# Performance work log

Hardware: AMD Instinct MI355X
Metric: run time of the kernel (lower is better)

The kernel has to match this reference:

```python
import jax, jax.numpy as jnp
import numpy as np

T, B, C = 2000, 32, 128   # frames, batch, classes (blank = 0)
L = 100                   # target length (fixed per batch)
W0, WLAST, THALF, NSTEP = 1.0, 0.1, 10000.0, 1
NEG_INF = -1e30

# ---- static STC graph (star-augmented CTC lattice) ----
# states: 0..2L  standard CTC lattice (even=blank, odd=target[(l-1)//2])
#         2L+1+l star node c_l for l=0..L  -> N = 3L+2
# arc label types: 0=blank, 1=target[lpos], 2=star_minus_target[lpos] (idx C+tgt), 3=full star (idx C)
# arc weight types: 0 -> 0, 1 -> log(wt), 2 -> 0 if target[wpos]!=target[wpos-1] else -inf (skip arc)

def _build_arcs(L):
    S = 2 * L + 1
    star = lambda l: S + l
    rows = []
    add = lambda s, d, lt, lp, wt, wp: rows.append((s, d, lt, lp, wt, wp))
    for l in range(S):
        idx = (l - 1) // 2
        if l % 2 == 0:
            add(l, l, 0, 0, 0, 0)              # blank self-loop
        if l > 0:
            if l % 2:
                add(l - 1, l, 1, idx, 0, 0)    # advance, emit target[idx]
            else:
                add(l - 1, l, 0, 0, 0, 0)      # advance, emit blank
        if l % 2 and l > 1:
            add(l - 2, l, 1, idx, 2, idx)      # skip arc (masked on repeats)
    for l in range(L + 1):
        p1, p2, c1 = 2 * l - 1, 2 * l, star(l)
        lt, lp = (3, 0) if l == L else (2, l)
        if p1 >= 0:
            add(p1, c1, lt, lp, 1, 0)
        add(p2, c1, lt, lp, 1, 0)
        add(c1, c1, lt, lp, 1, 0)              # star self-loop, weight log(wt)
        if l < L:
            add(c1, 2 * l + 1, 1, l, 0, 0)
        add(c1, p2, 0, 0, 0, 0)
    a = np.array(rows, dtype=np.int32).T
    return tuple(jnp.asarray(x) for x in a)

SRC, DST, LTYPE, LPOS, WTYPE, WPOS = _build_arcs(L)
N_STATES = 3 * L + 2
ACCEPT = jnp.array([2 * L - 1, 2 * L, 3 * L + 1])  # S-2, S-1, star c_L


def setup_inputs():
    key = jax.random.key(0)
    k1, k2 = jax.random.split(key)
    logits = jax.random.normal(k1, (T, B, C), dtype=jnp.float32)
    inputs = jax.nn.log_softmax(logits, axis=-1)          # [T, B, C] log-probs
    targets = jax.random.randint(k2, (B, L), 1, C, dtype=jnp.int32)
    return {"inputs": inputs, "targets": targets}


def _stc_loss(lp_aug, targets, logwt):
    # lp_aug: [B, T, 2C] augmented emissions; targets: [B, L]
    tgt = targets[:, LPOS]                                   # [B, A]
    labels = jnp.where(LTYPE == 0, 0,
             jnp.where(LTYPE == 1, tgt,
             jnp.where(LTYPE == 2, C + tgt, C)))             # [B, A] emission index
    prev = targets[:, jnp.maximum(WPOS - 1, 0)]
    w = jnp.where(WTYPE == 0, 0.0,
        jnp.where(WTYPE == 1, logwt,
        jnp.where(targets[:, WPOS] != prev, 0.0, NEG_INF)))  # [B, A]
    alpha0 = jnp.full((B, N_STATES), NEG_INF, dtype=lp_aug.dtype).at[:, 0].set(0.0)

    seg_max = jax.vmap(lambda s: jax.ops.segment_max(s, DST, num_segments=N_STATES))
    seg_sum = jax.vmap(lambda s: jax.ops.segment_sum(s, DST, num_segments=N_STATES))

    def step(alpha, emit_t):                                 # emit_t: [B, 2C]
        sc = alpha[:, SRC] + w + jnp.take_along_axis(emit_t, labels, axis=1)
        m = jnp.maximum(seg_max(sc), NEG_INF)                # stable scatter-logsumexp
        z = seg_sum(jnp.exp(sc - m[:, DST]))
        return m + jnp.log(z), None

    alpha, _ = jax.lax.scan(step, alpha0, jnp.swapaxes(lp_aug, 0, 1))
    score = jax.nn.logsumexp(alpha[:, ACCEPT], axis=1)       # forward score
    return jnp.mean(-score / T)                              # reduction='mean' then batch mean


def reference(inputs, targets):
    # wt schedule (nstep = 1 after one training step)
    wt = WLAST + (W0 - WLAST) * np.exp(-NSTEP * np.log(2.0) / THALF)
    lp = jnp.transpose(inputs, (1, 0, 2))                    # [B, T, C]
    lse = jax.nn.logsumexp(lp[:, :, 1:], axis=2, keepdims=True)
    neglse = lse + jnp.log1p(1e-7 - jnp.exp(lp[:, :, 1:] - lse))  # logsubexp
    lp_aug = jnp.concatenate([lp, lse, neglse], axis=2)      # [B, T, 2C]
    return _stc_loss(lp_aug, targets, float(np.log(wt)))
```

## Files before the change

### kernel.cpp

```cpp
#include <hip/hip_runtime.h>
#include <math.h>


#define T_LEN   2000
#define BATCH   32
#define NCLS    128
#define LTGT    100
#define CHUNK   16
#define EROWS   8
#define NEG_INF_F (-1e30f)

typedef float f32x4 __attribute__((ext_vector_type(4)));

#if __has_builtin(__builtin_amdgcn_exp2f)
#define EXP2(x) __builtin_amdgcn_exp2f(x)
#else
#define EXP2(x) exp2f(x)
#endif
#if __has_builtin(__builtin_amdgcn_logf)
#define LOG2(x) __builtin_amdgcn_logf(x)
#else
#define LOG2(x) __log2f(x)
#endif

__global__ void __launch_bounds__(64)
stc_emit(const float* __restrict__ inputs,
         const int*   __restrict__ targets,
         float4*      __restrict__ tabA,
         float*       __restrict__ tabB,
         const float wt)
{
    const int tbase = blockIdx.x * EROWS;
    const int b     = blockIdx.y;
    const int lane  = threadIdx.x;

    __shared__ float lps[EROWS][NCLS];

    int tg0 = 0, tg1 = 0;
    if (lane < 50) {
        tg0 = targets[b * LTGT + 2 * lane];
        tg1 = targets[b * LTGT + 2 * lane + 1];
    }
    const float L2E = 1.4426950408889634f;

#define ELD(i) const float2 x##i = *(const float2*)(inputs +                 \
                   ((size_t)(tbase + (i)) * BATCH + b) * NCLS + 2 * lane);
    ELD(0) ELD(1) ELD(2) ELD(3) ELD(4) ELD(5) ELD(6) ELD(7)
#undef ELD
#define EST(i) *(float2*)&lps[i][2 * lane] = x##i;
    EST(0) EST(1) EST(2) EST(3) EST(4) EST(5) EST(6) EST(7)
#undef EST
#define EPART(i) const float ex##i = __expf(x##i.x);                          \
                 float p##i = (lane == 0) ? __expf(x##i.y)                    \
                                          : ex##i + __expf(x##i.y);
    EPART(0) EPART(1) EPART(2) EPART(3) EPART(4) EPART(5) EPART(6) EPART(7)
#undef EPART
#define ERED(off) p0 += __shfl_xor(p0, off, 64); p1 += __shfl_xor(p1, off, 64);\
                  p2 += __shfl_xor(p2, off, 64); p3 += __shfl_xor(p3, off, 64);\
                  p4 += __shfl_xor(p4, off, 64); p5 += __shfl_xor(p5, off, 64);\
                  p6 += __shfl_xor(p6, off, 64); p7 += __shfl_xor(p7, off, 64);
    ERED(32) ERED(16) ERED(8) ERED(4) ERED(2) ERED(1)
#undef ERED
#define EPB(i) const float pb##i = __shfl(ex##i, 0, 64);
    EPB(0) EPB(1) EPB(2) EPB(3) EPB(4) EPB(5) EPB(6) EPB(7)
#undef EPB

    if (lane < 50) {
#define EOUT(i) do {                                                          \
        const float lt0 = lps[i][tg0], lt1 = lps[i][tg1];                     \
        const float aa  = fmaf(wt * (1.0f + 1e-7f), p##i, pb##i);             \
        const float q0  = fmaf(-wt, __expf(lt0), aa);                         \
        const float q1  = fmaf(-wt, __expf(lt1), aa);                         \
        tabA[((size_t)b * T_LEN + tbase + (i)) * 50 + lane] =                 \
            make_float4(L2E * lt0, L2E * lt1, LOG2(q0), LOG2(q1));            \
    } while (0);
        EOUT(0) EOUT(1) EOUT(2) EOUT(3) EOUT(4) EOUT(5) EOUT(6) EOUT(7)
#undef EOUT
    } else if (lane == 50) {
#define EOB(i) tabB[(size_t)b * T_LEN + tbase + (i)] =                        \
                   LOG2(fmaf(wt, p##i, pb##i));
        EOB(0) EOB(1) EOB(2) EOB(3) EOB(4) EOB(5) EOB(6) EOB(7)
#undef EOB
    }
}

__device__ __forceinline__ float shift_up1_ninf(float x)
{
    return __int_as_float(
        __builtin_amdgcn_update_dpp(__float_as_int(NEG_INF_F),
                                    __float_as_int(x), 0x138, 0xf, 0xf, false));
}
__device__ __forceinline__ float shift_dn1_ninf(float x)
{
    return __int_as_float(
        __builtin_amdgcn_update_dpp(__float_as_int(NEG_INF_F),
                                    __float_as_int(x), 0x130, 0xf, 0xf, false));
}

#define GL4(dst, base, imm)                                             \
    asm volatile("global_load_dwordx4 %0, %1, off offset:" #imm         \
                 : "=&v"(dst) : "v"(base))
#define VMWAIT(n) do {                                                  \
        asm volatile("s_waitcnt vmcnt(" #n ")" ::: "memory");           \
        __builtin_amdgcn_sched_barrier(0);                              \
    } while (0)

__global__ void __launch_bounds__(128, 1)
stc_scan(const float4* __restrict__ tabA,
         const float*  __restrict__ tabB,
         const int*    __restrict__ targets,
         float*        __restrict__ out)
{
    const int b    = blockIdx.x;
    const int lane = threadIdx.x & 63;
    const int wave = threadIdx.x >> 6;
    const bool l50 = (lane == 50);

    __shared__ float sb[4][64];

    const int tb0 = b * LTGT;
    const int c0 = 2 * lane, c1 = 2 * lane + 1;
    bool skb0 = false, skb1 = false;
    if (c0 >= 1 && c0 <= 99)
        skb0 = (targets[tb0 + c0] != targets[tb0 + c0 - 1]);
    if (c1 <= 99)
        skb1 = (targets[tb0 + c1] != targets[tb0 + c1 - 1]);

    const char* gAc = (const char*)tabA + (size_t)b * T_LEN * 800
                    + (size_t)lane * 16;
    const char* gQc = (const char*)(tabB + (size_t)b * T_LEN);

    asm volatile("s_waitcnt vmcnt(0) lgkmcnt(0)" ::: "memory");
    __builtin_amdgcn_sched_barrier(0);

    f32x4 Xv0, Xv1, Xv2, Xv3, Xv4, Xv5, Xv6, Xv7,
          Xv8, Xv9, Xv10, Xv11, Xv12, Xv13, Xv14, Xv15, Xq0, Xq1, Xq2, Xq3;
    f32x4 Yv0, Yv1, Yv2, Yv3, Yv4, Yv5, Yv6, Yv7,
          Yv8, Yv9, Yv10, Yv11, Yv12, Yv13, Yv14, Yv15, Yq0, Yq1, Yq2, Yq3;

#define LOADB(P, trow) do {                                             \
        const char* a0_ = gAc + (size_t)(trow) * 800;                   \
        const char* a1_ = a0_ + 4000;                                   \
        const char* a2_ = a0_ + 8000;                                   \
        GL4(P##v0,  a0_, 0);    GL4(P##v1,  a0_, 800);                  \
        GL4(P##v2,  a0_, 1600); GL4(P##v3,  a0_, 2400);                 \
        GL4(P##v4,  a0_, 3200);                                         \
        GL4(P##v5,  a1_, 0);    GL4(P##v6,  a1_, 800);                  \
        GL4(P##v7,  a1_, 1600); GL4(P##v8,  a1_, 2400);                 \
        GL4(P##v9,  a1_, 3200);                                         \
        GL4(P##v10, a2_, 0);    GL4(P##v11, a2_, 800);                  \
        GL4(P##v12, a2_, 1600); GL4(P##v13, a2_, 2400);                 \
        GL4(P##v14, a2_, 3200); GL4(P##v15, a2_, 4000);                 \
        const char* q_ = gQc + (size_t)(trow) * 4;                      \
        GL4(P##q0, q_, 0);  GL4(P##q1, q_, 16);                         \
        GL4(P##q2, q_, 32); GL4(P##q3, q_, 48);                         \
    } while (0)

    float A0 = (lane == 0) ? 0.0f : NEG_INF_F;
    float O0 = NEG_INF_F, A1 = NEG_INF_F, O1 = NEG_INF_F;
    float p0 = NEG_INF_F;

    if (wave == 0) {
#define FSTEP(vx, vy, vz, vw, qk) do {                                 \
        const float m1  = fmaxf(A1, O0);                               \
        const float lz1 = LOG2(1.0f + EXP2(-fabsf(A1 - O0)));          \
        const float O1n = skb1 ? (m1 + (vy)) + lz1 : A1 + (vy);        \
        const float psh = shift_up1_ninf(O1n);                         \
        A1 = (m1 + (vw)) + lz1;                                        \
        O1 = O1n;                                                      \
        const float m0  = fmaxf(A0, p0);                               \
        const float lz0 = LOG2(1.0f + EXP2(-fabsf(A0 - p0)));          \
        const float lq0 = l50 ? (qk) : (vz);                           \
        O0 = skb0 ? (m0 + (vx)) + lz0 : A0 + (vx);                     \
        A0 = (m0 + lq0) + lz0;                                         \
        p0 = psh;                                                      \
    } while (0)
#define RUNF(P) do {                                                       \
        FSTEP(P##v0[0],  P##v0[1],  P##v0[2],  P##v0[3],  P##q0[0]);       \
        FSTEP(P##v1[0],  P##v1[1],  P##v1[2],  P##v1[3],  P##q0[1]);       \
        FSTEP(P##v2[0],  P##v2[1],  P##v2[2],  P##v2[3],  P##q0[2]);       \
        FSTEP(P##v3[0],  P##v3[1],  P##v3[2],  P##v3[3],  P##q0[3]);       \
        FSTEP(P##v4[0],  P##v4[1],  P##v4[2],  P##v4[3],  P##q1[0]);       \
        FSTEP(P##v5[0],  P##v5[1],  P##v5[2],  P##v5[3],  P##q1[1]);       \
        FSTEP(P##v6[0],  P##v6[1],  P##v6[2],  P##v6[3],  P##q1[2]);       \
        FSTEP(P##v7[0],  P##v7[1],  P##v7[2],  P##v7[3],  P##q1[3]);       \
        FSTEP(P##v8[0],  P##v8[1],  P##v8[2],  P##v8[3],  P##q2[0]);       \
        FSTEP(P##v9[0],  P##v9[1],  P##v9[2],  P##v9[3],  P##q2[1]);       \
        FSTEP(P##v10[0], P##v10[1], P##v10[2], P##v10[3], P##q2[2]);       \
        FSTEP(P##v11[0], P##v11[1], P##v11[2], P##v11[3], P##q2[3]);       \
        FSTEP(P##v12[0], P##v12[1], P##v12[2], P##v12[3], P##q3[0]);       \
        FSTEP(P##v13[0], P##v13[1], P##v13[2], P##v13[3], P##q3[1]);       \
        FSTEP(P##v14[0], P##v14[1], P##v14[2], P##v14[3], P##q3[2]);       \
        FSTEP(P##v15[0], P##v15[1], P##v15[2], P##v15[3], P##q3[3]);       \
    } while (0)
        LOADB(X, 0);
        for (int c = 0; c + 1 < 63; c += 2) {
            LOADB(Y, 16 * (c + 1)); VMWAIT(20); RUNF(X);
            LOADB(X, 16 * (c + 2)); VMWAIT(20); RUNF(Y);
        }
        VMWAIT(0); RUNF(X);
#undef RUNF
#undef FSTEP
    } else {
        float bA0 = l50 ? 0.0f : NEG_INF_F;
        float bA1 = NEG_INF_F;
        float bO0 = NEG_INF_F;
        float bO1 = (lane == 49) ? 0.0f : NEG_INF_F;
#define BSTEP(vx, vy, vz, vw, qk) do {                                 \
        const float x1  = bA1 + (vw);                                  \
        const float y1  = bO1 + (vy);                                  \
        const float m1  = fmaxf(x1, y1);                               \
        const float lz1 = LOG2(1.0f + EXP2(-fabsf(x1 - y1)));          \
        const float L1  = m1 + lz1;                                    \
        const float lq0 = l50 ? (qk) : (vz);                           \
        const float x0  = bA0 + lq0;                                   \
        const float y0  = bO0 + (vx);                                  \
        const float m0  = fmaxf(x0, y0);                               \
        const float lz0 = LOG2(1.0f + EXP2(-fabsf(x0 - y0)));          \
        const float L0  = m0 + lz0;                                    \
        const float t0  = skb0 ? L0 : x0;                              \
        const float psh = shift_dn1_ninf(t0);       \
        bO0 = skb1 ? L1 : x1;                                          \
        bA0 = l50 ? x0 : L0;                                           \
        bA1 = L1;                                                      \
        bO1 = psh;                                                     \
    } while (0)
#define RUNBK(P) do {                                                      \
        BSTEP(P##v15[0], P##v15[1], P##v15[2], P##v15[3], P##q3[3]);       \
        BSTEP(P##v14[0], P##v14[1], P##v14[2], P##v14[3], P##q3[2]);       \
        BSTEP(P##v13[0], P##v13[1], P##v13[2], P##v13[3], P##q3[1]);       \
        BSTEP(P##v12[0], P##v12[1], P##v12[2], P##v12[3], P##q3[0]);       \
        BSTEP(P##v11[0], P##v11[1], P##v11[2], P##v11[3], P##q2[3]);       \
        BSTEP(P##v10[0], P##v10[1], P##v10[2], P##v10[3], P##q2[2]);       \
        BSTEP(P##v9[0],  P##v9[1],  P##v9[2],  P##v9[3],  P##q2[1]);       \
        BSTEP(P##v8[0],  P##v8[1],  P##v8[2],  P##v8[3],  P##q2[0]);       \
        BSTEP(P##v7[0],  P##v7[1],  P##v7[2],  P##v7[3],  P##q1[3]);       \
        BSTEP(P##v6[0],  P##v6[1],  P##v6[2],  P##v6[3],  P##q1[2]);       \
        BSTEP(P##v5[0],  P##v5[1],  P##v5[2],  P##v5[3],  P##q1[1]);       \
        BSTEP(P##v4[0],  P##v4[1],  P##v4[2],  P##v4[3],  P##q1[0]);       \
        BSTEP(P##v3[0],  P##v3[1],  P##v3[2],  P##v3[3],  P##q0[3]);       \
        BSTEP(P##v2[0],  P##v2[1],  P##v2[2],  P##v2[3],  P##q0[2]);       \
        BSTEP(P##v1[0],  P##v1[1],  P##v1[2],  P##v1[3],  P##q0[1]);       \
        BSTEP(P##v0[0],  P##v0[1],  P##v0[2],  P##v0[3],  P##q0[0]);       \
    } while (0)
        LOADB(X, 1984);
        for (int k = 0; k + 1 < 61; k += 2) {
            LOADB(Y, 1984 - 16 * (k + 1)); VMWAIT(20); RUNBK(X);
            LOADB(X, 1984 - 16 * (k + 2)); VMWAIT(20); RUNBK(Y);
        }
        LOADB(Y, 1008); VMWAIT(20); RUNBK(X);
        VMWAIT(0); RUNBK(Y);
#undef RUNBK
#undef BSTEP
        sb[0][lane] = bA0; sb[1][lane] = bA1;
        sb[2][lane] = bO0; sb[3][lane] = bO1;
    }
#undef LOADB

    __syncthreads();

    if (wave == 0) {
        const float bA0g = sb[0][lane], bA1g = sb[1][lane];
        const float bO0g = sb[2][lane], bO1g = sb[3][lane];
        const float T0 = (lane <= 50) ? A0 + bA0g : NEG_INF_F;
        const float T1 = (lane < 50)  ? A1 + bA1g : NEG_INF_F;
        const float T2 = (lane < 50)  ? O0 + bO0g : NEG_INF_F;
        const float T3 = (lane < 50)  ? O1 + bO1g : NEG_INF_F;
        float M = fmaxf(fmaxf(T0, T1), fmaxf(T2, T3));
        float S = EXP2(T0 - M) + EXP2(T1 - M) + EXP2(T2 - M) + EXP2(T3 - M);
        #pragma unroll
        for (int off = 32; off >= 1; off >>= 1) {
            const float Mo = __shfl_xor(M, off, 64);
            const float So = __shfl_xor(S, off, 64);
            const float Mn = fmaxf(M, Mo);
            S = S * EXP2(M - Mn) + So * EXP2(Mo - Mn);
            M = Mn;
        }
        if (lane == 0) {
            const float LN2 = 0.6931471805599453f;
            atomicAdd(out, -(M + LOG2(S)) * LN2
                               / ((float)T_LEN * (float)BATCH));
        }
    }
}

extern "C" void kernel_launch(void* const* d_in, const int* in_sizes, int n_in,
                              void* d_out, int out_size, void* d_ws, size_t ws_size,
                              hipStream_t stream)
{
    const float* inputs  = (const float*)d_in[0];
    const int*   targets = (const int*)d_in[1];
    float*       out     = (float*)d_out;

    float4* tabA = (float4*)d_ws;
    float*  tabB = (float*)((char*)d_ws + (size_t)BATCH * T_LEN * 50 * 16);

    const float wt = (float)(0.1 + 0.9 * exp(-log(2.0) / 10000.0));

    (void)hipMemsetAsync(out, 0, sizeof(float), stream);
    stc_emit<<<dim3(T_LEN / EROWS, BATCH), dim3(64), 0, stream>>>(
        inputs, targets, tabA, tabB, wt);
    stc_scan<<<dim3(BATCH), dim3(128), 0, stream>>>(tabA, tabB, targets, out);
}
```

Baseline: 138.5 us.

## Fuse emission precompute into scan kernel with producer waves and LDS double buffer

The separate emission kernel and its global-memory tables are removed. A single 256-thread block per batch item now runs two producer waves, one per direction, that load raw log-probs, compute the augmented emissions, and write them into a double-buffered LDS staging area. Two consumer waves run the forward and backward recursions, reading their 16-step chunk from LDS. This avoids the second launch and the write and re-read of the large intermediate tables. In exchange it adds a block-wide barrier per chunk, and producer compute or load latency now sits on the critical path of the serial scan.

```diff
diff --git a/kernel.cpp b/kernel.cpp
--- a/kernel.cpp
+++ b/kernel.cpp
@@ -6,11 +6,10 @@
 #define BATCH   32
 #define NCLS    128
 #define LTGT    100
-#define CHUNK   16
-#define EROWS   8
 #define NEG_INF_F (-1e30f)
 
 typedef float f32x4 __attribute__((ext_vector_type(4)));
+typedef float f32x2 __attribute__((ext_vector_type(2)));
 
 #if __has_builtin(__builtin_amdgcn_exp2f)
 #define EXP2(x) __builtin_amdgcn_exp2f(x)
@@ -23,67 +22,6 @@
 #define LOG2(x) __log2f(x)
 #endif
 
-__global__ void __launch_bounds__(64)
-stc_emit(const float* __restrict__ inputs,
-         const int*   __restrict__ targets,
-         float4*      __restrict__ tabA,
-         float*       __restrict__ tabB,
-         const float wt)
-{
-    const int tbase = blockIdx.x * EROWS;
-    const int b     = blockIdx.y;
-    const int lane  = threadIdx.x;
-
-    __shared__ float lps[EROWS][NCLS];
-
-    int tg0 = 0, tg1 = 0;
-    if (lane < 50) {
-        tg0 = targets[b * LTGT + 2 * lane];
-        tg1 = targets[b * LTGT + 2 * lane + 1];
-    }
-    const float L2E = 1.4426950408889634f;
-
-#define ELD(i) const float2 x##i = *(const float2*)(inputs +                 \
-                   ((size_t)(tbase + (i)) * BATCH + b) * NCLS + 2 * lane);
-    ELD(0) ELD(1) ELD(2) ELD(3) ELD(4) ELD(5) ELD(6) ELD(7)
-#undef ELD
-#define EST(i) *(float2*)&lps[i][2 * lane] = x##i;
-    EST(0) EST(1) EST(2) EST(3) EST(4) EST(5) EST(6) EST(7)
-#undef EST
-#define EPART(i) const float ex##i = __expf(x##i.x);                          \
-                 float p##i = (lane == 0) ? __expf(x##i.y)                    \
-                                          : ex##i + __expf(x##i.y);
-    EPART(0) EPART(1) EPART(2) EPART(3) EPART(4) EPART(5) EPART(6) EPART(7)
-#undef EPART
-#define ERED(off) p0 += __shfl_xor(p0, off, 64); p1 += __shfl_xor(p1, off, 64);\
-                  p2 += __shfl_xor(p2, off, 64); p3 += __shfl_xor(p3, off, 64);\
-                  p4 += __shfl_xor(p4, off, 64); p5 += __shfl_xor(p5, off, 64);\
-                  p6 += __shfl_xor(p6, off, 64); p7 += __shfl_xor(p7, off, 64);
-    ERED(32) ERED(16) ERED(8) ERED(4) ERED(2) ERED(1)
-#undef ERED
-#define EPB(i) const float pb##i = __shfl(ex##i, 0, 64);
-    EPB(0) EPB(1) EPB(2) EPB(3) EPB(4) EPB(5) EPB(6) EPB(7)
-#undef EPB
-
-    if (lane < 50) {
-#define EOUT(i) do {                                                          \
-        const float lt0 = lps[i][tg0], lt1 = lps[i][tg1];                     \
-        const float aa  = fmaf(wt * (1.0f + 1e-7f), p##i, pb##i);             \
-        const float q0  = fmaf(-wt, __expf(lt0), aa);                         \
-        const float q1  = fmaf(-wt, __expf(lt1), aa);                         \
-        tabA[((size_t)b * T_LEN + tbase + (i)) * 50 + lane] =                 \
-            make_float4(L2E * lt0, L2E * lt1, LOG2(q0), LOG2(q1));            \
-    } while (0);
-        EOUT(0) EOUT(1) EOUT(2) EOUT(3) EOUT(4) EOUT(5) EOUT(6) EOUT(7)
-#undef EOUT
-    } else if (lane == 50) {
-#define EOB(i) tabB[(size_t)b * T_LEN + tbase + (i)] =                        \
-                   LOG2(fmaf(wt, p##i, pb##i));
-        EOB(0) EOB(1) EOB(2) EOB(3) EOB(4) EOB(5) EOB(6) EOB(7)
-#undef EOB
-    }
-}
-
 __device__ __forceinline__ float shift_up1_ninf(float x)
 {
     return __int_as_float(
@@ -97,25 +35,41 @@
                                     __float_as_int(x), 0x130, 0xf, 0xf, false));
 }
 
-#define GL4(dst, base, imm)                                             \
-    asm volatile("global_load_dwordx4 %0, %1, off offset:" #imm         \
+__device__ __forceinline__ unsigned ldsa(const void* p)
+{
+    return (unsigned)(unsigned long long)
+        (const __attribute__((address_space(3))) char*)p;
+}
+
+#define GL2(dst, base)                                                  \
+    asm volatile("global_load_dwordx2 %0, %1, off"                      \
                  : "=&v"(dst) : "v"(base))
+#define DSR4(dst, addr, imm)                                            \
+    asm volatile("ds_read_b128 %0, %1 offset:" #imm                     \
+                 : "=&v"(dst) : "v"(addr))
 #define VMWAIT(n) do {                                                  \
         asm volatile("s_waitcnt vmcnt(" #n ")" ::: "memory");           \
         __builtin_amdgcn_sched_barrier(0);                              \
     } while (0)
-
-__global__ void __launch_bounds__(128, 1)
-stc_scan(const float4* __restrict__ tabA,
-         const float*  __restrict__ tabB,
-         const int*    __restrict__ targets,
-         float*        __restrict__ out)
+#define LGKMWAIT() do {                                                 \
+        asm volatile("s_waitcnt lgkmcnt(0)" ::: "memory");              \
+        __builtin_amdgcn_sched_barrier(0);                              \
+    } while (0)
+
+__global__ void __launch_bounds__(256, 1)
+stc_fused(const float* __restrict__ inputs,
+          const int*   __restrict__ targets,
+          float*       __restrict__ out,
+          const float wt)
 {
     const int b    = blockIdx.x;
     const int lane = threadIdx.x & 63;
     const int wave = threadIdx.x >> 6;
     const bool l50 = (lane == 50);
 
+    __shared__ float4 emisA[2][2][16][64];
+    __shared__ __align__(16) float emisQ[2][2][16];
+    __shared__ float lps[2][16][NCLS];
     __shared__ float sb[4][64];
 
     const int tb0 = b * LTGT;
@@ -125,42 +79,122 @@
         skb0 = (targets[tb0 + c0] != targets[tb0 + c0 - 1]);
     if (c1 <= 99)
         skb1 = (targets[tb0 + c1] != targets[tb0 + c1 - 1]);
-
-    const char* gAc = (const char*)tabA + (size_t)b * T_LEN * 800
-                    + (size_t)lane * 16;
-    const char* gQc = (const char*)(tabB + (size_t)b * T_LEN);
-
-    asm volatile("s_waitcnt vmcnt(0) lgkmcnt(0)" ::: "memory");
-    __builtin_amdgcn_sched_barrier(0);
-
-    f32x4 Xv0, Xv1, Xv2, Xv3, Xv4, Xv5, Xv6, Xv7,
-          Xv8, Xv9, Xv10, Xv11, Xv12, Xv13, Xv14, Xv15, Xq0, Xq1, Xq2, Xq3;
-    f32x4 Yv0, Yv1, Yv2, Yv3, Yv4, Yv5, Yv6, Yv7,
-          Yv8, Yv9, Yv10, Yv11, Yv12, Yv13, Yv14, Yv15, Yq0, Yq1, Yq2, Yq3;
-
-#define LOADB(P, trow) do {                                             \
-        const char* a0_ = gAc + (size_t)(trow) * 800;                   \
-        const char* a1_ = a0_ + 4000;                                   \
-        const char* a2_ = a0_ + 8000;                                   \
-        GL4(P##v0,  a0_, 0);    GL4(P##v1,  a0_, 800);                  \
-        GL4(P##v2,  a0_, 1600); GL4(P##v3,  a0_, 2400);                 \
-        GL4(P##v4,  a0_, 3200);                                         \
-        GL4(P##v5,  a1_, 0);    GL4(P##v6,  a1_, 800);                  \
-        GL4(P##v7,  a1_, 1600); GL4(P##v8,  a1_, 2400);                 \
-        GL4(P##v9,  a1_, 3200);                                         \
-        GL4(P##v10, a2_, 0);    GL4(P##v11, a2_, 800);                  \
-        GL4(P##v12, a2_, 1600); GL4(P##v13, a2_, 2400);                 \
-        GL4(P##v14, a2_, 3200); GL4(P##v15, a2_, 4000);                 \
-        const char* q_ = gQc + (size_t)(trow) * 4;                      \
-        GL4(P##q0, q_, 0);  GL4(P##q1, q_, 16);                         \
-        GL4(P##q2, q_, 32); GL4(P##q3, q_, 48);                         \
-    } while (0)
+    int tg0 = 0, tg1 = 0;
+    if (lane < 50) {
+        tg0 = targets[tb0 + c0];
+        tg1 = targets[tb0 + c1];
+    }
+
+    const float L2E = 1.4426950408889634f;
+    const float wtp = wt * (1.0f + 1e-7f);
+    const char* inSrc = (const char*)inputs + (size_t)b * 512
+                      + (size_t)lane * 8;
+
+    {
+        const float4 z4 = make_float4(0.f, 0.f, 0.f, 0.f);
+        float4* ea = (float4*)emisA;
+        for (int i = threadIdx.x; i < 2 * 2 * 16 * 64; i += 256) ea[i] = z4;
+        float* eq = (float*)emisQ;
+        if (threadIdx.x < 64) eq[threadIdx.x] = 0.f;
+    }
+
+#define PTROW(dir, c) ((dir) ? (1984 - 16 * (c)) : (16 * (c)))
+#define LOADP(S, trow) do {                                             \
+        const char* p_ = inSrc + (size_t)(trow) * 16384;                \
+        GL2(S##0,  p_);            GL2(S##1,  p_ + 16384);              \
+        GL2(S##2,  p_ + 32768);    GL2(S##3,  p_ + 49152);              \
+        GL2(S##4,  p_ + 65536);    GL2(S##5,  p_ + 81920);              \
+        GL2(S##6,  p_ + 98304);    GL2(S##7,  p_ + 114688);             \
+        GL2(S##8,  p_ + 131072);   GL2(S##9,  p_ + 147456);             \
+        GL2(S##10, p_ + 163840);   GL2(S##11, p_ + 180224);             \
+        GL2(S##12, p_ + 196608);   GL2(S##13, p_ + 212992);             \
+        GL2(S##14, p_ + 229376);   GL2(S##15, p_ + 245760);             \
+    } while (0)
+
+#define PROW(i, X, dir, bi) do {                                        \
+        *(float2*)&lps[dir][i][2 * lane] = make_float2(X[0], X[1]);     \
+        const float ex_ = __expf(X[0]);                                 \
+        float ps_ = (lane == 0) ? __expf(X[1]) : ex_ + __expf(X[1]);    \
+        ps_ += __shfl_xor(ps_, 32, 64);                                 \
+        ps_ += __shfl_xor(ps_, 16, 64);                                 \
+        ps_ += __shfl_xor(ps_, 8, 64);                                  \
+        ps_ += __shfl_xor(ps_, 4, 64);                                  \
+        ps_ += __shfl_xor(ps_, 2, 64);                                  \
+        ps_ += __shfl_xor(ps_, 1, 64);                                  \
+        const float pb_ = __shfl(ex_, 0, 64);                           \
+        if (lane < 50) {                                                \
+            const float lt0_ = lps[dir][i][tg0];                        \
+            const float lt1_ = lps[dir][i][tg1];                        \
+            const float aa_  = fmaf(wtp, ps_, pb_);                     \
+            const float q0_  = fmaf(-wt, __expf(lt0_), aa_);            \
+            const float q1_  = fmaf(-wt, __expf(lt1_), aa_);            \
+            emisA[dir][bi][i][lane] =                                   \
+                make_float4(L2E * lt0_, L2E * lt1_, LOG2(q0_), LOG2(q1_)); \
+        } else if (lane == 50) {                                        \
+            emisQ[dir][bi][i] = LOG2(fmaf(wt, ps_, pb_));               \
+        }                                                               \
+    } while (0)
+
+#define PROWS(S, dir, bi) do {                                          \
+        PROW(0,  S##0,  dir, bi); PROW(1,  S##1,  dir, bi);             \
+        PROW(2,  S##2,  dir, bi); PROW(3,  S##3,  dir, bi);             \
+        PROW(4,  S##4,  dir, bi); PROW(5,  S##5,  dir, bi);             \
+        PROW(6,  S##6,  dir, bi); PROW(7,  S##7,  dir, bi);             \
+        PROW(8,  S##8,  dir, bi); PROW(9,  S##9,  dir, bi);             \
+        PROW(10, S##10, dir, bi); PROW(11, S##11, dir, bi);             \
+        PROW(12, S##12, dir, bi); PROW(13, S##13, dir, bi);             \
+        PROW(14, S##14, dir, bi); PROW(15, S##15, dir, bi);             \
+    } while (0)
+
+    f32x2 eA0, eA1, eA2, eA3, eA4, eA5, eA6, eA7,
+          eA8, eA9, eA10, eA11, eA12, eA13, eA14, eA15;
+    f32x2 eB0, eB1, eB2, eB3, eB4, eB5, eB6, eB7,
+          eB8, eB9, eB10, eB11, eB12, eB13, eB14, eB15;
+
+    const int pdir  = wave - 2;
+    const int plast = (wave == 3) ? 61 : 62;
+
+    if (wave >= 2) {
+        LOADP(eA, PTROW(pdir, 0));
+        LOADP(eB, PTROW(pdir, 1));
+    }
+
+    __syncthreads();
+
+    if (wave >= 2) {
+        VMWAIT(16);
+        PROWS(eA, pdir, 0);
+    }
+
+    __syncthreads();
 
     float A0 = (lane == 0) ? 0.0f : NEG_INF_F;
     float O0 = NEG_INF_F, A1 = NEG_INF_F, O1 = NEG_INF_F;
     float p0 = NEG_INF_F;
-
-    if (wave == 0) {
+    float bA0 = l50 ? 0.0f : NEG_INF_F;
+    float bA1 = NEG_INF_F;
+    float bO0 = NEG_INF_F;
+    float bO1 = (lane == 49) ? 0.0f : NEG_INF_F;
+
+    f32x4 Xv0, Xv1, Xv2, Xv3, Xv4, Xv5, Xv6, Xv7,
+          Xv8, Xv9, Xv10, Xv11, Xv12, Xv13, Xv14, Xv15, Xq0, Xq1, Xq2, Xq3;
+
+#define STAGEC(dir, bi) do {                                            \
+        const unsigned a_ = ldsa(&emisA[dir][bi][0][lane]);             \
+        DSR4(Xv0,  a_, 0);     DSR4(Xv1,  a_, 1024);                    \
+        DSR4(Xv2,  a_, 2048);  DSR4(Xv3,  a_, 3072);                    \
+        DSR4(Xv4,  a_, 4096);  DSR4(Xv5,  a_, 5120);                    \
+        DSR4(Xv6,  a_, 6144);  DSR4(Xv7,  a_, 7168);                    \
+        DSR4(Xv8,  a_, 8192);  DSR4(Xv9,  a_, 9216);                    \
+        DSR4(Xv10, a_, 10240); DSR4(Xv11, a_, 11264);                   \
+        DSR4(Xv12, a_, 12288); DSR4(Xv13, a_, 13312);                   \
+        DSR4(Xv14, a_, 14336); DSR4(Xv15, a_, 15360);                   \
+        const unsigned q_ = ldsa(&emisQ[dir][bi][0]);                   \
+        DSR4(Xq0, q_, 0);  DSR4(Xq1, q_, 16);                           \
+        DSR4(Xq2, q_, 32); DSR4(Xq3, q_, 48);                           \
+        LGKMWAIT();                                                     \
+    } while (0)
+
 #define FSTEP(vx, vy, vz, vw, qk) do {                                 \
         const float m1  = fmaxf(A1, O0);                               \
         const float lz1 = LOG2(1.0f + EXP2(-fabsf(A1 - O0)));          \
@@ -175,37 +209,25 @@
         A0 = (m0 + lq0) + lz0;                                         \
         p0 = psh;                                                      \
     } while (0)
-#define RUNF(P) do {                                                       \
-        FSTEP(P##v0[0],  P##v0[1],  P##v0[2],  P##v0[3],  P##q0[0]);       \
-        FSTEP(P##v1[0],  P##v1[1],  P##v1[2],  P##v1[3],  P##q0[1]);       \
-        FSTEP(P##v2[0],  P##v2[1],  P##v2[2],  P##v2[3],  P##q0[2]);       \
-        FSTEP(P##v3[0],  P##v3[1],  P##v3[2],  P##v3[3],  P##q0[3]);       \
-        FSTEP(P##v4[0],  P##v4[1],  P##v4[2],  P##v4[3],  P##q1[0]);       \
-        FSTEP(P##v5[0],  P##v5[1],  P##v5[2],  P##v5[3],  P##q1[1]);       \
-        FSTEP(P##v6[0],  P##v6[1],  P##v6[2],  P##v6[3],  P##q1[2]);       \
-        FSTEP(P##v7[0],  P##v7[1],  P##v7[2],  P##v7[3],  P##q1[3]);       \
-        FSTEP(P##v8[0],  P##v8[1],  P##v8[2],  P##v8[3],  P##q2[0]);       \
-        FSTEP(P##v9[0],  P##v9[1],  P##v9[2],  P##v9[3],  P##q2[1]);       \
-        FSTEP(P##v10[0], P##v10[1], P##v10[2], P##v10[3], P##q2[2]);       \
-        FSTEP(P##v11[0], P##v11[1], P##v11[2], P##v11[3], P##q2[3]);       \
-        FSTEP(P##v12[0], P##v12[1], P##v12[2], P##v12[3], P##q3[0]);       \
-        FSTEP(P##v13[0], P##v13[1], P##v13[2], P##v13[3], P##q3[1]);       \
-        FSTEP(P##v14[0], P##v14[1], P##v14[2], P##v14[3], P##q3[2]);       \
-        FSTEP(P##v15[0], P##v15[1], P##v15[2], P##v15[3], P##q3[3]);       \
-    } while (0)
-        LOADB(X, 0);
-        for (int c = 0; c + 1 < 63; c += 2) {
-            LOADB(Y, 16 * (c + 1)); VMWAIT(20); RUNF(X);
-            LOADB(X, 16 * (c + 2)); VMWAIT(20); RUNF(Y);
-        }
-        VMWAIT(0); RUNF(X);
-#undef RUNF
-#undef FSTEP
-    } else {
-        float bA0 = l50 ? 0.0f : NEG_INF_F;
-        float bA1 = NEG_INF_F;
-        float bO0 = NEG_INF_F;
-        float bO1 = (lane == 49) ? 0.0f : NEG_INF_F;
+#define RUNF() do {                                                        \
+        FSTEP(Xv0[0],  Xv0[1],  Xv0[2],  Xv0[3],  Xq0[0]);                 \
+        FSTEP(Xv1[0],  Xv1[1],  Xv1[2],  Xv1[3],  Xq0[1]);                 \
+        FSTEP(Xv2[0],  Xv2[1],  Xv2[2],  Xv2[3],  Xq0[2]);                 \
+        FSTEP(Xv3[0],  Xv3[1],  Xv3[2],  Xv3[3],  Xq0[3]);                 \
+        FSTEP(Xv4[0],  Xv4[1],  Xv4[2],  Xv4[3],  Xq1[0]);                 \
+        FSTEP(Xv5[0],  Xv5[1],  Xv5[2],  Xv5[3],  Xq1[1]);                 \
+        FSTEP(Xv6[0],  Xv6[1],  Xv6[2],  Xv6[3],  Xq1[2]);                 \
+        FSTEP(Xv7[0],  Xv7[1],  Xv7[2],  Xv7[3],  Xq1[3]);                 \
+        FSTEP(Xv8[0],  Xv8[1],  Xv8[2],  Xv8[3],  Xq2[0]);                 \
+        FSTEP(Xv9[0],  Xv9[1],  Xv9[2],  Xv9[3],  Xq2[1]);                 \
+        FSTEP(Xv10[0], Xv10[1], Xv10[2], Xv10[3], Xq2[2]);                 \
+        FSTEP(Xv11[0], Xv11[1], Xv11[2], Xv11[3], Xq2[3]);                 \
+        FSTEP(Xv12[0], Xv12[1], Xv12[2], Xv12[3], Xq3[0]);                 \
+        FSTEP(Xv13[0], Xv13[1], Xv13[2], Xv13[3], Xq3[1]);                 \
+        FSTEP(Xv14[0], Xv14[1], Xv14[2], Xv14[3], Xq3[2]);                 \
+        FSTEP(Xv15[0], Xv15[1], Xv15[2], Xv15[3], Xq3[3]);                 \
+    } while (0)
+
 #define BSTEP(vx, vy, vz, vw, qk) do {                                 \
         const float x1  = bA1 + (vw);                                  \
         const float y1  = bO1 + (vy);                                  \
@@ -225,38 +247,56 @@
         bA1 = L1;                                                      \
         bO1 = psh;                                                     \
     } while (0)
-#define RUNBK(P) do {                                                      \
-        BSTEP(P##v15[0], P##v15[1], P##v15[2], P##v15[3], P##q3[3]);       \
-        BSTEP(P##v14[0], P##v14[1], P##v14[2], P##v14[3], P##q3[2]);       \
-        BSTEP(P##v13[0], P##v13[1], P##v13[2], P##v13[3], P##q3[1]);       \
-        BSTEP(P##v12[0], P##v12[1], P##v12[2], P##v12[3], P##q3[0]);       \
-        BSTEP(P##v11[0], P##v11[1], P##v11[2], P##v11[3], P##q2[3]);       \
-        BSTEP(P##v10[0], P##v10[1], P##v10[2], P##v10[3], P##q2[2]);       \
-        BSTEP(P##v9[0],  P##v9[1],  P##v9[2],  P##v9[3],  P##q2[1]);       \
-        BSTEP(P##v8[0],  P##v8[1],  P##v8[2],  P##v8[3],  P##q2[0]);       \
-        BSTEP(P##v7[0],  P##v7[1],  P##v7[2],  P##v7[3],  P##q1[3]);       \
-        BSTEP(P##v6[0],  P##v6[1],  P##v6[2],  P##v6[3],  P##q1[2]);       \
-        BSTEP(P##v5[0],  P##v5[1],  P##v5[2],  P##v5[3],  P##q1[1]);       \
-        BSTEP(P##v4[0],  P##v4[1],  P##v4[2],  P##v4[3],  P##q1[0]);       \
-        BSTEP(P##v3[0],  P##v3[1],  P##v3[2],  P##v3[3],  P##q0[3]);       \
-        BSTEP(P##v2[0],  P##v2[1],  P##v2[2],  P##v2[3],  P##q0[2]);       \
-        BSTEP(P##v1[0],  P##v1[1],  P##v1[2],  P##v1[3],  P##q0[1]);       \
-        BSTEP(P##v0[0],  P##v0[1],  P##v0[2],  P##v0[3],  P##q0[0]);       \
-    } while (0)
-        LOADB(X, 1984);
-        for (int k = 0; k + 1 < 61; k += 2) {
-            LOADB(Y, 1984 - 16 * (k + 1)); VMWAIT(20); RUNBK(X);
-            LOADB(X, 1984 - 16 * (k + 2)); VMWAIT(20); RUNBK(Y);
+#define RUNBK() do {                                                       \
+        BSTEP(Xv15[0], Xv15[1], Xv15[2], Xv15[3], Xq3[3]);                 \
+        BSTEP(Xv14[0], Xv14[1], Xv14[2], Xv14[3], Xq3[2]);                 \
+        BSTEP(Xv13[0], Xv13[1], Xv13[2], Xv13[3], Xq3[1]);                 \
+        BSTEP(Xv12[0], Xv12[1], Xv12[2], Xv12[3], Xq3[0]);                 \
+        BSTEP(Xv11[0], Xv11[1], Xv11[2], Xv11[3], Xq2[3]);                 \
+        BSTEP(Xv10[0], Xv10[1], Xv10[2], Xv10[3], Xq2[2]);                 \
+        BSTEP(Xv9[0],  Xv9[1],  Xv9[2],  Xv9[3],  Xq2[1]);                 \
+        BSTEP(Xv8[0],  Xv8[1],  Xv8[2],  Xv8[3],  Xq2[0]);                 \
+        BSTEP(Xv7[0],  Xv7[1],  Xv7[2],  Xv7[3],  Xq1[3]);                 \
+        BSTEP(Xv6[0],  Xv6[1],  Xv6[2],  Xv6[3],  Xq1[2]);                 \
+        BSTEP(Xv5[0],  Xv5[1],  Xv5[2],  Xv5[3],  Xq1[1]);                 \
+        BSTEP(Xv4[0],  Xv4[1],  Xv4[2],  Xv4[3],  Xq1[0]);                 \
+        BSTEP(Xv3[0],  Xv3[1],  Xv3[2],  Xv3[3],  Xq0[3]);                 \
+        BSTEP(Xv2[0],  Xv2[1],  Xv2[2],  Xv2[3],  Xq0[2]);                 \
+        BSTEP(Xv1[0],  Xv1[1],  Xv1[2],  Xv1[3],  Xq0[1]);                 \
+        BSTEP(Xv0[0],  Xv0[1],  Xv0[2],  Xv0[3],  Xq0[0]);                 \
+    } while (0)
+
+    for (int k = 0; k < 63; ++k) {
+        if (wave == 0) {
+            STAGEC(0, (k & 1));
+            RUNF();
+        } else if (wave == 1) {
+            if (k < 62) {
+                STAGEC(1, (k & 1));
+                RUNBK();
+            }
+        } else {
+            const int c = k + 1;
+            if (c <= plast) {
+                const int cn = c + 1;
+                if (cn <= plast) {
+                    if (cn & 1) { LOADP(eB, PTROW(pdir, cn)); }
+                    else        { LOADP(eA, PTROW(pdir, cn)); }
+                    VMWAIT(16);
+                } else {
+                    VMWAIT(0);
+                }
+                if (c & 1) PROWS(eB, pdir, (c & 1));
+                else       PROWS(eA, pdir, (c & 1));
+            }
         }
-        LOADB(Y, 1008); VMWAIT(20); RUNBK(X);
-        VMWAIT(0); RUNBK(Y);
-#undef RUNBK
-#undef BSTEP
+        __syncthreads();
+    }
+
+    if (wave == 1) {
         sb[0][lane] = bA0; sb[1][lane] = bA1;
         sb[2][lane] = bO0; sb[3][lane] = bO1;
     }
-#undef LOADB
-
     __syncthreads();
 
     if (wave == 0) {
@@ -291,14 +331,10 @@
     const float* inputs  = (const float*)d_in[0];
     const int*   targets = (const int*)d_in[1];
     float*       out     = (float*)d_out;
-
-    float4* tabA = (float4*)d_ws;
-    float*  tabB = (float*)((char*)d_ws + (size_t)BATCH * T_LEN * 50 * 16);
+    (void)d_ws; (void)ws_size;
 
     const float wt = (float)(0.1 + 0.9 * exp(-log(2.0) / 10000.0));
 
     (void)hipMemsetAsync(out, 0, sizeof(float), stream);
-    stc_emit<<<dim3(T_LEN / EROWS, BATCH), dim3(64), 0, stream>>>(
-        inputs, targets, tabA, tabB, wt);
-    stc_scan<<<dim3(BATCH), dim3(128), 0, stream>>>(tabA, tabB, targets, out);
-}
+    stc_fused<<<dim3(BATCH), dim3(256), 0, stream>>>(inputs, targets, out, wt);
+}
```

New measurement: 395.5 us. 186% more time.
